# Optimization experiments

Measured on AMD Instinct MI355X. Metric: run time of the kernel, lower is better.

The kernel has to match this reference:

```python
import jax, jax.numpy as jnp
import numpy as np

# Multi-scale deformable attention (MSDeformAttn) with the pytorch grid_sample
# fallback semantics: bilinear, padding_mode='zeros', align_corners=False.
SPATIAL_SHAPES = [(128, 128), (64, 64), (32, 32), (16, 16)]  # (H_l, W_l)
N, C, M, L, P = 2, 256, 8, 4, 4
D = C // M
LEN_IN = sum(h * w for h, w in SPATIAL_SHAPES)  # 21760


def setup_inputs() -> dict:
    key = jax.random.key(0)
    ks = jax.random.split(key, 11)
    s = 0.02
    return {
        "query": jax.random.normal(ks[0], (N, LEN_IN, C), jnp.float32),
        "reference_points": jax.random.uniform(ks[1], (N, LEN_IN, L, 2), jnp.float32),
        "input_flatten": jax.random.normal(ks[2], (N, LEN_IN, C), jnp.float32),
        "W_off": jax.random.normal(ks[3], (C, M * L * P * 2), jnp.float32) * s,
        "b_off": jax.random.normal(ks[4], (M * L * P * 2,), jnp.float32) * s,
        "W_attn": jax.random.normal(ks[5], (C, M * L * P), jnp.float32) * s,
        "b_attn": jax.random.normal(ks[6], (M * L * P,), jnp.float32) * s,
        "W_val": jax.random.normal(ks[7], (C, C), jnp.float32) * s,
        "b_val": jax.random.normal(ks[8], (C,), jnp.float32) * s,
        "W_out": jax.random.normal(ks[9], (C, C), jnp.float32) * s,
        "b_out": jax.random.normal(ks[10], (C,), jnp.float32) * s,
    }


def _bilinear_sample(val_flat, gx, gy, H, W):
    """grid_sample(bilinear, zeros, align_corners=False) on one level.
    val_flat: (N, M, H*W, D); gx, gy: (N, M, Lq*P) in [-1, 1] (any value)."""
    x = (gx + 1.0) * (W * 0.5) - 0.5
    y = (gy + 1.0) * (H * 0.5) - 0.5
    x0 = jnp.floor(x)
    y0 = jnp.floor(y)
    wx1 = x - x0  # fractional parts
    wy1 = y - y0
    x0i = x0.astype(jnp.int32)
    y0i = y0.astype(jnp.int32)

    def gather(ix, iy):
        valid = (ix >= 0) & (ix < W) & (iy >= 0) & (iy < H)
        idx = jnp.clip(iy, 0, H - 1) * W + jnp.clip(ix, 0, W - 1)
        g = jnp.take_along_axis(val_flat, idx[..., None], axis=2)  # (N,M,LqP,D)
        return g * valid[..., None].astype(val_flat.dtype)

    g00 = gather(x0i, y0i)
    g01 = gather(x0i + 1, y0i)
    g10 = gather(x0i, y0i + 1)
    g11 = gather(x0i + 1, y0i + 1)
    return (g00 * ((1 - wx1) * (1 - wy1))[..., None]
            + g01 * (wx1 * (1 - wy1))[..., None]
            + g10 * ((1 - wx1) * wy1)[..., None]
            + g11 * (wx1 * wy1)[..., None])


def reference(query, reference_points, input_flatten, W_off, b_off,
              W_attn, b_attn, W_val, b_val, W_out, b_out):
    Nq, Lq, _ = query.shape
    # value projection -> (N, Len_in, M, D)
    value = (input_flatten @ W_val + b_val).reshape(Nq, -1, M, D)
    # sampling offsets -> (N, Lq, M, L, P, 2)
    offsets = (query @ W_off + b_off).reshape(Nq, Lq, M, L, P, 2)
    # attention weights: softmax over L*P
    attn = jax.nn.softmax((query @ W_attn + b_attn).reshape(Nq, Lq, M, L * P), axis=-1)
    attn = attn.reshape(Nq, Lq, M, L, P)
    # offset normalizer is (W_l, H_l)
    norm = jnp.array([[w, h] for h, w in SPATIAL_SHAPES], jnp.float32)  # (L, 2)
    loc = reference_points[:, :, None, :, None, :] + offsets / norm[None, None, None, :, None, :]
    grid = 2.0 * loc - 1.0  # (N, Lq, M, L, P, 2)

    acc = jnp.zeros((Nq, M, Lq, D), value.dtype)
    start = 0
    for lvl, (H, W) in enumerate(SPATIAL_SHAPES):
        val_flat = value[:, start:start + H * W].transpose(0, 2, 1, 3)  # (N,M,HW,D)
        gx = grid[:, :, :, lvl, :, 0].transpose(0, 2, 1, 3).reshape(Nq, M, Lq * P)
        gy = grid[:, :, :, lvl, :, 1].transpose(0, 2, 1, 3).reshape(Nq, M, Lq * P)
        samp = _bilinear_sample(val_flat, gx, gy, H, W).reshape(Nq, M, Lq, P, D)
        w_l = attn[:, :, :, lvl, :].transpose(0, 2, 1, 3)  # (N, M, Lq, P)
        acc = acc + jnp.einsum('nmqpd,nmqp->nmqd', samp, w_l)
        start += H * W

    out = acc.transpose(0, 2, 1, 3).reshape(Nq, Lq, C)  # (N, Lq, C)
    return out @ W_out + b_out
```

## Files before the change

kernel.cpp:

```cpp
#include <hip/hip_runtime.h>
#include <hip/hip_fp16.h>
#include <math.h>
#include <stdint.h>


constexpr int NB  = 2;
constexpr int C   = 256;
constexpr int M   = 8;
constexpr int D   = 32;
constexpr int LEN = 21760;
constexpr int QCHc = LEN / 2;

typedef __attribute__((ext_vector_type(8))) short short8v;
typedef __attribute__((ext_vector_type(4))) float f32x4;

__device__ __forceinline__ short f2bf(float x) {
  uint32_t u = __float_as_uint(x);
  u = (u + 0x7fffu + ((u >> 16) & 1u)) >> 16;
  return (short)u;
}

__global__ __launch_bounds__(256) void k_wpack(
    const float* __restrict__ Wval, const float* __restrict__ Woff,
    const float* __restrict__ Wattn, const float* __restrict__ Wout,
    short* __restrict__ WvP, short* __restrict__ WdP, short* __restrict__ WoP) {
  const int job = blockIdx.y;
  const int ncols = (job == 1) ? 384 : 256;
  const int NCG = ncols / 16;
  const int elems = 256 * ncols;
  const int idx = blockIdx.x * 256 + threadIdx.x;
  if (idx >= elems) return;
  const int e    = idx & 7;
  const int lane = (idx >> 3) & 63;
  const int lr = lane & 15, lk = lane >> 4;
  const int cgks = idx >> 9;
  const int cg = cgks % NCG, ks = cgks / NCG;
  const int k = ks * 32 + lk * 8 + e;
  const int col = cg * 16 + lr;
  float v;
  if (job == 0)      v = Wval[(size_t)k * 256 + col];
  else if (job == 2) v = Wout[(size_t)k * 256 + col];
  else               v = (col < 256) ? Woff[(size_t)k * 256 + col]
                                     : Wattn[(size_t)k * 128 + col - 256];
  short* dst = (job == 0) ? WvP : (job == 1) ? WdP : WoP;
  dst[idx] = f2bf(v);
}

__device__ __forceinline__ short8v ldBP(const short* __restrict__ WP, int NCG,
                                        int cg, int ks, int lane) {
  const int4 v = *(const int4*)(WP + ((size_t)((ks * NCG + cg) * 64 + lane)) * 8);
  union { int4 i; short8v s; } u; u.i = v; return u.s;
}

__device__ __forceinline__ void stage_cast(const float* __restrict__ p, char* sm, int t) {
  const int r = t >> 3, seg = t & 7;
  const float4* s = (const float4*)(p + (size_t)r * C + seg * 32);
  short v[32];
#pragma unroll
  for (int i = 0; i < 8; ++i) {
    float4 f = s[i];
    v[i * 4 + 0] = f2bf(f.x); v[i * 4 + 1] = f2bf(f.y);
    v[i * 4 + 2] = f2bf(f.z); v[i * 4 + 3] = f2bf(f.w);
  }
#pragma unroll
  for (int i = 0; i < 4; ++i) {
    const int kb = (seg * 32 + i * 8) * 2;
    *(int4*)(sm + r * 512 + (kb ^ ((r & 7) << 4))) = ((const int4*)v)[i];
  }
}

__device__ __forceinline__ void stage_bf16(const short* __restrict__ p, char* sm, int t) {
  const int r = t >> 3, seg = t & 7;
  const int4* s = (const int4*)(p + (size_t)r * C + seg * 32);
#pragma unroll
  for (int i = 0; i < 4; ++i) {
    const int kb = (seg * 32 + i * 8) * 2;
    *(int4*)(sm + r * 512 + (kb ^ ((r & 7) << 4))) = s[i];
  }
}

__device__ __forceinline__ short8v ldsA(const char* sm, int lane, int rt, int ks) {
  const int row = rt * 16 + (lane & 15);
  const int kb  = ks * 64 + ((lane >> 4) << 4);
  const int4 v = *(const int4*)(sm + row * 512 + (kb ^ ((row & 7) << 4)));
  union { int4 i; short8v s; } u; u.i = v; return u.s;
}

#define MFMA __builtin_amdgcn_mfma_f32_16x16x32_bf16

#define GEMM_BODY(WP)                                                       \
  short8v a[2][8];                                                          \
  _Pragma("unroll") for (int rt = 0; rt < 2; ++rt)                          \
  _Pragma("unroll") for (int ks = 0; ks < 8; ++ks)                          \
      a[rt][ks] = ldsA(smA, lane, rt, ks);                                  \
  f32x4 acc[2][4];                                                          \
  _Pragma("unroll") for (int rt = 0; rt < 2; ++rt)                          \
  _Pragma("unroll") for (int ct = 0; ct < 4; ++ct)                          \
      acc[rt][ct] = (f32x4){0.f, 0.f, 0.f, 0.f};                            \
  short8v b0[8], b1[8];                                                     \
  _Pragma("unroll") for (int ks = 0; ks < 8; ++ks)                          \
      b0[ks] = ldBP(WP, 16, cg0 + 0, ks, lane);                             \
  _Pragma("unroll") for (int ks = 0; ks < 8; ++ks)                          \
      b1[ks] = ldBP(WP, 16, cg0 + 1, ks, lane);                             \
  _Pragma("unroll") for (int ks = 0; ks < 8; ++ks) {                        \
    acc[0][0] = MFMA(a[0][ks], b0[ks], acc[0][0], 0, 0, 0);                 \
    acc[1][0] = MFMA(a[1][ks], b0[ks], acc[1][0], 0, 0, 0);                 \
  }                                                                         \
  _Pragma("unroll") for (int ks = 0; ks < 8; ++ks)                          \
      b0[ks] = ldBP(WP, 16, cg0 + 2, ks, lane);                             \
  _Pragma("unroll") for (int ks = 0; ks < 8; ++ks) {                        \
    acc[0][1] = MFMA(a[0][ks], b1[ks], acc[0][1], 0, 0, 0);                 \
    acc[1][1] = MFMA(a[1][ks], b1[ks], acc[1][1], 0, 0, 0);                 \
  }                                                                         \
  _Pragma("unroll") for (int ks = 0; ks < 8; ++ks)                          \
      b1[ks] = ldBP(WP, 16, cg0 + 3, ks, lane);                             \
  _Pragma("unroll") for (int ks = 0; ks < 8; ++ks) {                        \
    acc[0][2] = MFMA(a[0][ks], b0[ks], acc[0][2], 0, 0, 0);                 \
    acc[1][2] = MFMA(a[1][ks], b0[ks], acc[1][2], 0, 0, 0);                 \
  }                                                                         \
  _Pragma("unroll") for (int ks = 0; ks < 8; ++ks) {                        \
    acc[0][3] = MFMA(a[0][ks], b1[ks], acc[0][3], 0, 0, 0);                 \
    acc[1][3] = MFMA(a[1][ks], b1[ks], acc[1][3], 0, 0, 0);                 \
  }

__global__ __launch_bounds__(256, 2) void k_valproj(
    const float* __restrict__ infl, const short* __restrict__ WvP,
    const float* __restrict__ bv, __half* __restrict__ value) {
  __shared__ __align__(16) char smA[16384];
  const int t = threadIdx.x, lane = t & 63, w = t >> 6;
  const int r0 = blockIdx.x * 32;
  stage_cast(infl + (size_t)r0 * C, smA, t);
  __syncthreads();
  const int cg0 = w * 4;
  const int lr = lane & 15, lk = lane >> 4;
  GEMM_BODY(WvP)

  const int n = (blockIdx.x >= (LEN / 32)) ? 1 : 0;
  const int pixbase = r0 - n * LEN;
#pragma unroll
  for (int ct = 0; ct < 4; ++ct) {
    const int col = (cg0 + ct) * 16 + lr;
    const float bb = bv[col];
    const int m = col >> 5, d = col & 31;
    __half* vp = value + ((size_t)(n * 8 + m) * LEN) * 32 + d;
#pragma unroll
    for (int rt = 0; rt < 2; ++rt)
#pragma unroll
      for (int r = 0; r < 4; ++r) {
        const int pix = pixbase + rt * 16 + lk * 4 + r;
        vp[(size_t)pix * 32] = __float2half(acc[rt][ct][r] + bb);
      }
  }
}

__global__ __launch_bounds__(256, 2) void k_outproj(
    const short* __restrict__ accB, const short* __restrict__ WoP,
    const float* __restrict__ bo, float* __restrict__ out) {
  __shared__ __align__(16) char smA[16384];
  const int t = threadIdx.x, lane = t & 63, w = t >> 6;
  const int r0 = blockIdx.x * 32;
  stage_bf16(accB + (size_t)r0 * C, smA, t);
  __syncthreads();
  const int cg0 = w * 4;
  const int lr = lane & 15, lk = lane >> 4;
  GEMM_BODY(WoP)

#pragma unroll
  for (int ct = 0; ct < 4; ++ct) {
    const int col = (cg0 + ct) * 16 + lr;
    const float bb = bo[col];
#pragma unroll
    for (int rt = 0; rt < 2; ++rt)
#pragma unroll
      for (int r = 0; r < 4; ++r) {
        const int row = r0 + rt * 16 + lk * 4 + r;
        out[(size_t)row * C + col] = acc[rt][ct][r] + bb;
      }
  }
}

__global__ __launch_bounds__(256, 3) void k_desc(
    const float* __restrict__ query, const float* __restrict__ refp,
    const short* __restrict__ WdP, const float* __restrict__ boff,
    const float* __restrict__ battn, uint2* __restrict__ descD, int qbase) {
  __shared__ __align__(16) char smem[50176];
  char*  smA  = smem;
  float* offs = (float*)smem;
  float* attw = (float*)(smem + 32768);
  float* refs = (float*)(smem + 49152);

  const int t = threadIdx.x, lane = t & 63, w = t >> 6;
  const int n   = blockIdx.x / 340;
  const int q0c = (blockIdx.x % 340) * 32;
  const size_t qrow = (size_t)n * LEN + qbase + q0c;

  refs[t] = refp[qrow * 8 + t];
  stage_cast(query + qrow * C, smA, t);
  __syncthreads();

  f32x4 acc[2][6];
#pragma unroll
  for (int a = 0; a < 2; ++a)
#pragma unroll
    for (int b = 0; b < 6; ++b) acc[a][b] = (f32x4){0.f, 0.f, 0.f, 0.f};
  const int cgb = w * 6;
#pragma unroll
  for (int ks = 0; ks < 8; ++ks) {
    const short8v a0 = ldsA(smA, lane, 0, ks);
    const short8v a1 = ldsA(smA, lane, 1, ks);
#pragma unroll
    for (int ct = 0; ct < 6; ++ct) {
      const short8v b = ldBP(WdP, 24, cgb + ct, ks, lane);
      acc[0][ct] = MFMA(a0, b, acc[0][ct], 0, 0, 0);
      acc[1][ct] = MFMA(a1, b, acc[1][ct], 0, 0, 0);
    }
  }
  __syncthreads();

#pragma unroll
  for (int ct = 0; ct < 6; ++ct) {
    const int col = (cgb + ct) * 16 + (lane & 15);
    const float bb = (col < 256) ? boff[col] : battn[col - 256];
#pragma unroll
    for (int rt = 0; rt < 2; ++rt)
#pragma unroll
      for (int r = 0; r < 4; ++r) {
        const int row = rt * 16 + ((lane >> 4) << 2) + r;
        const float vv = acc[rt][ct][r] + bb;
        if (col < 256) offs[row * 256 + col] = vv;
        else           attw[row * 128 + col - 256] = vv;
      }
  }
  __syncthreads();

  {
    const int q = t >> 3, m = t & 7;
    float v[16], mx = -1e30f;
#pragma unroll
    for (int j = 0; j < 16; ++j) { v[j] = attw[q * 128 + m * 16 + j]; mx = fmaxf(mx, v[j]); }
    float s = 0.f;
#pragma unroll
    for (int j = 0; j < 16; ++j) { v[j] = __expf(v[j] - mx); s += v[j]; }
    const float inv = 1.f / s;
#pragma unroll
    for (int j = 0; j < 16; ++j) attw[q * 128 + m * 16 + j] = v[j] * inv;
  }
  __syncthreads();

#pragma unroll
  for (int i = 0; i < 16; ++i) {
    const int e = i * 256 + t;
    const int q = e >> 7, rem = e & 127;
    const int m = rem >> 4, j = rem & 15, l = j >> 2;
    const int jo = m * 16 + j;
    const float ox = offs[q * 256 + 2 * jo], oy = offs[q * 256 + 2 * jo + 1];
    const float aw = attw[q * 128 + jo];
    const float rx = refs[q * 8 + l * 2 + 0], ry = refs[q * 8 + l * 2 + 1];
    const int W = 128 >> l;
    const float x = rx * (float)W + ox - 0.5f;
    const float y = ry * (float)W + oy - 0.5f;
    const float xc = fminf(fmaxf(x, -8.f), 503.f);
    const float yc = fminf(fmaxf(y, -8.f), 503.f);
    const uint32_t xfix = (uint32_t)((xc + 8.f) * 128.f + 0.5f);
    const uint32_t yfix = (uint32_t)((yc + 8.f) * 128.f + 0.5f);
    uint2 dsc;
    dsc.x = xfix | (yfix << 16);
    dsc.y = (uint32_t)__half_as_ushort(__float2half_rn(aw));
    descD[((size_t)(n * 8 + m) * QCHc + q0c + q) * 16 + j] = dsc;
  }
}

__global__ __launch_bounds__(256, 4) void k_gather(
    const uint2* __restrict__ descD, const __half* __restrict__ value,
    short* __restrict__ accB, int qbase) {
  const int t = threadIdx.x;
  const int d4 = t & 3, ql = t >> 2;
  const int bid = blockIdx.x;
  const int s = bid & 15, qc = bid >> 4;
  const int n = s >> 3, m = s & 7;
  const int q = qc * 64 + ql;
  const uint4* dp4 = (const uint4*)(descD + ((size_t)(n * 8 + m) * QCHc + q) * 16);
  const char* vb = (const char*)value +
                   (size_t)((n * 8 + m) * LEN) * 64 + d4 * 16;

  uint4 dd[8];
#pragma unroll
  for (int i = 0; i < 8; ++i) dd[i] = dp4[i];
  __builtin_amdgcn_sched_barrier(0);

  float accf[8];
#pragma unroll
  for (int i = 0; i < 8; ++i) accf[i] = 0.f;

  union V { uint4 v; __half2 h[4]; };
  V rA[8], rB[8];
  __half2 hwA[8], hwB[8];

#define DECJ(G, ODD, R, HW, BASE)                                             \
  {                                                                           \
    constexpr int l_ = (G) >> 1;                                              \
    constexpr int W_ = 128 >> l_;                                             \
    constexpr int stl_ = (l_ == 0) ? 0 : (l_ == 1) ? 16384 : (l_ == 2) ? 20480 : 21504; \
    const uint32_t lo_ = (ODD) ? dd[G].z : dd[G].x;                           \
    const uint32_t hi_ = (ODD) ? dd[G].w : dd[G].y;                           \
    const int xf_ = (int)(lo_ & 0xffffu), yf_ = (int)(lo_ >> 16);             \
    const float aw_ = __half2float(__ushort_as_half((unsigned short)(hi_ & 0xffffu))); \
    const int xi_ = (xf_ >> 7) - 8, yi_ = (yf_ >> 7) - 8;                     \
    const float fx_ = (float)(xf_ & 127) * 0.0078125f;                        \
    const float fy_ = (float)(yf_ & 127) * 0.0078125f;                        \
    float wx0_ = 1.f - fx_, wx1_ = fx_, wy0_ = 1.f - fy_, wy1_ = fy_;         \
    if (xi_ < 0 || xi_ >= W_)         wx0_ = 0.f;                             \
    if (xi_ + 1 < 0 || xi_ + 1 >= W_) wx1_ = 0.f;                             \
    if (yi_ < 0 || yi_ >= W_)         wy0_ = 0.f;                             \
    if (yi_ + 1 < 0 || yi_ + 1 >= W_) wy1_ = 0.f;                             \
    const int x0_ = min(max(xi_, 0), W_ - 1), x1_ = min(max(xi_ + 1, 0), W_ - 1); \
    const int y0_ = min(max(yi_, 0), W_ - 1), y1_ = min(max(yi_ + 1, 0), W_ - 1); \
    HW[(BASE) + 0] = __float2half2_rn(wx0_ * wy0_ * aw_);                     \
    HW[(BASE) + 1] = __float2half2_rn(wx1_ * wy0_ * aw_);                     \
    HW[(BASE) + 2] = __float2half2_rn(wx0_ * wy1_ * aw_);                     \
    HW[(BASE) + 3] = __float2half2_rn(wx1_ * wy1_ * aw_);                     \
    R[(BASE) + 0].v = *(const uint4*)(vb + (size_t)(stl_ + y0_ * W_ + x0_) * 64u); \
    R[(BASE) + 1].v = *(const uint4*)(vb + (size_t)(stl_ + y0_ * W_ + x1_) * 64u); \
    R[(BASE) + 2].v = *(const uint4*)(vb + (size_t)(stl_ + y1_ * W_ + x0_) * 64u); \
    R[(BASE) + 3].v = *(const uint4*)(vb + (size_t)(stl_ + y1_ * W_ + x1_) * 64u); \
  }

#define DECG(G, R, HW)                                                        \
  DECJ(G, 0, R, HW, 0)                                                        \
  DECJ(G, 1, R, HW, 4)                                                        \
  __builtin_amdgcn_sched_barrier(0);

#define CONSG(R, HW)                                                          \
  {                                                                           \
    __half2 acch[4];                                                          \
    _Pragma("unroll") for (int i_ = 0; i_ < 4; ++i_)                          \
        acch[i_] = __float2half2_rn(0.f);                                     \
    _Pragma("unroll") for (int c_ = 0; c_ < 8; ++c_) {                        \
      _Pragma("unroll") for (int i_ = 0; i_ < 4; ++i_)                        \
          acch[i_] = __hfma2(R[c_].h[i_], HW[c_], acch[i_]);                  \
    }                                                                         \
    _Pragma("unroll") for (int i_ = 0; i_ < 4; ++i_) {                        \
      const float2 f_ = __half22float2(acch[i_]);                             \
      accf[2 * i_] += f_.x; accf[2 * i_ + 1] += f_.y;                         \
    }                                                                         \
  }

  DECG(0, rA, hwA)
  DECG(1, rB, hwB)
  CONSG(rA, hwA)
  DECG(2, rA, hwA)
  CONSG(rB, hwB)
  DECG(3, rB, hwB)
  CONSG(rA, hwA)
  DECG(4, rA, hwA)
  CONSG(rB, hwB)
  DECG(5, rB, hwB)
  CONSG(rA, hwA)
  DECG(6, rA, hwA)
  CONSG(rB, hwB)
  DECG(7, rB, hwB)
  CONSG(rA, hwA)
  CONSG(rB, hwB)
#undef DECJ
#undef DECG
#undef CONSG

  short8v o;
#pragma unroll
  for (int i = 0; i < 8; ++i) o[i] = f2bf(accf[i]);
  *(short8v*)(accB + ((size_t)n * LEN + qbase + q) * 256 + m * 32 + d4 * 8) = o;
}

extern "C" void kernel_launch(void* const* d_in, const int* in_sizes, int n_in,
                              void* d_out, int out_size, void* d_ws, size_t ws_size,
                              hipStream_t stream) {
  const float* query = (const float*)d_in[0];
  const float* refp  = (const float*)d_in[1];
  const float* infl  = (const float*)d_in[2];
  const float* Woff  = (const float*)d_in[3];
  const float* boff  = (const float*)d_in[4];
  const float* Wattn = (const float*)d_in[5];
  const float* battn = (const float*)d_in[6];
  const float* Wval  = (const float*)d_in[7];
  const float* bval  = (const float*)d_in[8];
  const float* Wout  = (const float*)d_in[9];
  const float* bout  = (const float*)d_in[10];
  float* out = (float*)d_out;

  char* ws = (char*)d_ws;
  __half* value = (__half*)ws;
  short*  accB  = (short*)(ws + 22282240);
  uint2*  desc8 = (uint2*)(ws + 44564480);
  short*  WvP   = (short*)(ws + 66846720);
  short*  WdP   = (short*)(ws + 66977792);
  short*  WoP   = (short*)(ws + 67174400);

  k_wpack<<<dim3(384, 3), 256, 0, stream>>>(Wval, Woff, Wattn, Wout,
                                            WvP, WdP, WoP);

  k_valproj<<<(NB * LEN) / 32, 256, 0, stream>>>(infl, WvP, bval, value);

  for (int c = 0; c < 2; ++c) {
    k_desc<<<NB * (QCHc / 32), 256, 0, stream>>>(query, refp, WdP, boff, battn,
                                                 desc8, c * QCHc);
    k_gather<<<16 * (QCHc / 64), 256, 0, stream>>>(desc8, value, accB, c * QCHc);
  }

  k_outproj<<<(NB * LEN) / 32, 256, 0, stream>>>(accB, WoP, bout, out);
}
```

Measured before the change: 156.8 us.

## Pad value maps with a zero border to drop bilinear bounds checks

Value projection now writes each level's feature map into a buffer with a one-pixel zero border, filled by a new k_zpad kernel. The descriptor builder clamps coordinates to [-1, W] instead of [-8, 503], so the gather kernel can drop the per-corner validity tests and index clamping. Each sample now loads two adjacent pixel pairs at fixed offsets from one base address. This cuts ALU work in the gather loop, in exchange for an extra small launch, a slightly larger value buffer, and scattered store addresses in valproj.

```diff
diff --git a/kernel.cpp b/kernel.cpp
--- a/kernel.cpp
+++ b/kernel.cpp
@@ -10,6 +10,7 @@
 constexpr int D   = 32;
 constexpr int LEN = 21760;
 constexpr int QCHc = LEN / 2;
+constexpr int PADPIX = 22736;
 
 typedef __attribute__((ext_vector_type(8))) short short8v;
 typedef __attribute__((ext_vector_type(4))) float f32x4;
@@ -44,6 +45,23 @@
                                      : Wattn[(size_t)k * 128 + col - 256];
   short* dst = (job == 0) ? WvP : (job == 1) ? WdP : WoP;
   dst[idx] = f2bf(v);
+}
+
+__global__ __launch_bounds__(256) void k_zpad(__half* __restrict__ value) {
+  const int s = blockIdx.x, l = blockIdx.y;
+  const int Wp  = (l == 0) ? 130 : (l == 1) ? 66 : (l == 2) ? 34 : 18;
+  const int stp = (l == 0) ? 0 : (l == 1) ? 16900 : (l == 2) ? 21256 : 22412;
+  const int cells = 4 * Wp - 4;
+  const uint4 z = {0u, 0u, 0u, 0u};
+  char* base = (char*)value + (size_t)s * PADPIX * 64;
+  for (int i = threadIdx.x; i < cells * 4; i += 256) {
+    const int cell = i >> 2, d4 = i & 3;
+    int row, col;
+    if (cell < Wp)            { row = 0;       col = cell; }
+    else if (cell < 2 * Wp)   { row = Wp - 1;  col = cell - Wp; }
+    else { const int c2 = cell - 2 * Wp; row = 1 + (c2 >> 1); col = (c2 & 1) ? (Wp - 1) : 0; }
+    *(uint4*)(base + (size_t)(stp + row * Wp + col) * 64 + d4 * 16) = z;
+  }
 }
 
 __device__ __forceinline__ short8v ldBP(const short* __restrict__ WP, int NCG,
@@ -137,19 +155,32 @@
 
   const int n = (blockIdx.x >= (LEN / 32)) ? 1 : 0;
   const int pixbase = r0 - n * LEN;
+
+  int pidx8[2][4];
+#pragma unroll
+  for (int rt = 0; rt < 2; ++rt)
+#pragma unroll
+    for (int r = 0; r < 4; ++r) {
+      const int pix = pixbase + rt * 16 + lk * 4 + r;
+      int pi;
+      if (pix < 16384)      { const int y = pix >> 7;           pi = (y + 1) * 130 + (pix & 127) + 1; }
+      else if (pix < 20480) { const int y = (pix - 16384) >> 6; pi = 16900 + (y + 1) * 66 + (pix & 63) + 1; }
+      else if (pix < 21504) { const int y = (pix - 20480) >> 5; pi = 21256 + (y + 1) * 34 + (pix & 31) + 1; }
+      else                  { const int y = (pix - 21504) >> 4; pi = 22412 + (y + 1) * 18 + (pix & 15) + 1; }
+      pidx8[rt][r] = pi;
+    }
+
 #pragma unroll
   for (int ct = 0; ct < 4; ++ct) {
     const int col = (cg0 + ct) * 16 + lr;
     const float bb = bv[col];
     const int m = col >> 5, d = col & 31;
-    __half* vp = value + ((size_t)(n * 8 + m) * LEN) * 32 + d;
+    __half* vp = value + ((size_t)(n * 8 + m) * PADPIX) * 32 + d;
 #pragma unroll
     for (int rt = 0; rt < 2; ++rt)
 #pragma unroll
-      for (int r = 0; r < 4; ++r) {
-        const int pix = pixbase + rt * 16 + lk * 4 + r;
-        vp[(size_t)pix * 32] = __float2half(acc[rt][ct][r] + bb);
-      }
+      for (int r = 0; r < 4; ++r)
+        vp[(size_t)pidx8[rt][r] * 32] = __float2half(acc[rt][ct][r] + bb);
   }
 }
 
@@ -257,12 +288,13 @@
     const float aw = attw[q * 128 + jo];
     const float rx = refs[q * 8 + l * 2 + 0], ry = refs[q * 8 + l * 2 + 1];
     const int W = 128 >> l;
-    const float x = rx * (float)W + ox - 0.5f;
-    const float y = ry * (float)W + oy - 0.5f;
-    const float xc = fminf(fmaxf(x, -8.f), 503.f);
-    const float yc = fminf(fmaxf(y, -8.f), 503.f);
-    const uint32_t xfix = (uint32_t)((xc + 8.f) * 128.f + 0.5f);
-    const uint32_t yfix = (uint32_t)((yc + 8.f) * 128.f + 0.5f);
+    const float fW = (float)W;
+    const float x = rx * fW + ox - 0.5f;
+    const float y = ry * fW + oy - 0.5f;
+    const float xc = fminf(fmaxf(x, -1.f), fW);
+    const float yc = fminf(fmaxf(y, -1.f), fW);
+    const uint32_t xfix = (uint32_t)((xc + 1.f) * 128.f + 0.5f);
+    const uint32_t yfix = (uint32_t)((yc + 1.f) * 128.f + 0.5f);
     uint2 dsc;
     dsc.x = xfix | (yfix << 16);
     dsc.y = (uint32_t)__half_as_ushort(__float2half_rn(aw));
@@ -281,7 +313,7 @@
   const int q = qc * 64 + ql;
   const uint4* dp4 = (const uint4*)(descD + ((size_t)(n * 8 + m) * QCHc + q) * 16);
   const char* vb = (const char*)value +
-                   (size_t)((n * 8 + m) * LEN) * 64 + d4 * 16;
+                   (size_t)((n * 8 + m)) * PADPIX * 64 + d4 * 16;
 
   uint4 dd[8];
 #pragma unroll
@@ -300,29 +332,28 @@
   {                                                                           \
     constexpr int l_ = (G) >> 1;                                              \
     constexpr int W_ = 128 >> l_;                                             \
-    constexpr int stl_ = (l_ == 0) ? 0 : (l_ == 1) ? 16384 : (l_ == 2) ? 20480 : 21504; \
+    constexpr int Wp_ = W_ + 2;                                               \
+    constexpr int stp_ = (l_ == 0) ? 0 : (l_ == 1) ? 16900 : (l_ == 2) ? 21256 : 22412; \
     const uint32_t lo_ = (ODD) ? dd[G].z : dd[G].x;                           \
     const uint32_t hi_ = (ODD) ? dd[G].w : dd[G].y;                           \
     const int xf_ = (int)(lo_ & 0xffffu), yf_ = (int)(lo_ >> 16);             \
     const float aw_ = __half2float(__ushort_as_half((unsigned short)(hi_ & 0xffffu))); \
-    const int xi_ = (xf_ >> 7) - 8, yi_ = (yf_ >> 7) - 8;                     \
+    const int xi_ = xf_ >> 7, yi_ = yf_ >> 7;                                 \
     const float fx_ = (float)(xf_ & 127) * 0.0078125f;                        \
     const float fy_ = (float)(yf_ & 127) * 0.0078125f;                        \
-    float wx0_ = 1.f - fx_, wx1_ = fx_, wy0_ = 1.f - fy_, wy1_ = fy_;         \
-    if (xi_ < 0 || xi_ >= W_)         wx0_ = 0.f;                             \
-    if (xi_ + 1 < 0 || xi_ + 1 >= W_) wx1_ = 0.f;                             \
-    if (yi_ < 0 || yi_ >= W_)         wy0_ = 0.f;                             \
-    if (yi_ + 1 < 0 || yi_ + 1 >= W_) wy1_ = 0.f;                             \
-    const int x0_ = min(max(xi_, 0), W_ - 1), x1_ = min(max(xi_ + 1, 0), W_ - 1); \
-    const int y0_ = min(max(yi_, 0), W_ - 1), y1_ = min(max(yi_ + 1, 0), W_ - 1); \
-    HW[(BASE) + 0] = __float2half2_rn(wx0_ * wy0_ * aw_);                     \
-    HW[(BASE) + 1] = __float2half2_rn(wx1_ * wy0_ * aw_);                     \
-    HW[(BASE) + 2] = __float2half2_rn(wx0_ * wy1_ * aw_);                     \
-    HW[(BASE) + 3] = __float2half2_rn(wx1_ * wy1_ * aw_);                     \
-    R[(BASE) + 0].v = *(const uint4*)(vb + (size_t)(stl_ + y0_ * W_ + x0_) * 64u); \
-    R[(BASE) + 1].v = *(const uint4*)(vb + (size_t)(stl_ + y0_ * W_ + x1_) * 64u); \
-    R[(BASE) + 2].v = *(const uint4*)(vb + (size_t)(stl_ + y1_ * W_ + x0_) * 64u); \
-    R[(BASE) + 3].v = *(const uint4*)(vb + (size_t)(stl_ + y1_ * W_ + x1_) * 64u); \
+    const float wx0_ = 1.f - fx_;                                             \
+    const float wy0a_ = (1.f - fy_) * aw_;                                    \
+    const float wy1a_ = fy_ * aw_;                                            \
+    HW[(BASE) + 0] = __float2half2_rn(wx0_ * wy0a_);                          \
+    HW[(BASE) + 1] = __float2half2_rn(fx_ * wy0a_);                           \
+    HW[(BASE) + 2] = __float2half2_rn(wx0_ * wy1a_);                          \
+    HW[(BASE) + 3] = __float2half2_rn(fx_ * wy1a_);                           \
+    const char* a0_ = vb + (size_t)(stp_ + yi_ * Wp_ + xi_) * 64u;            \
+    const char* a1_ = a0_ + Wp_ * 64;                                         \
+    R[(BASE) + 0].v = *(const uint4*)(a0_);                                   \
+    R[(BASE) + 1].v = *(const uint4*)(a0_ + 64);                              \
+    R[(BASE) + 2].v = *(const uint4*)(a1_);                                   \
+    R[(BASE) + 3].v = *(const uint4*)(a1_ + 64);                              \
   }
 
 #define DECG(G, R, HW)                                                        \
@@ -389,14 +420,15 @@
 
   char* ws = (char*)d_ws;
   __half* value = (__half*)ws;
-  short*  accB  = (short*)(ws + 22282240);
-  uint2*  desc8 = (uint2*)(ws + 44564480);
-  short*  WvP   = (short*)(ws + 66846720);
-  short*  WdP   = (short*)(ws + 66977792);
-  short*  WoP   = (short*)(ws + 67174400);
+  short*  accB  = (short*)(ws + 23281664);
+  uint2*  desc8 = (uint2*)(ws + 45563904);
+  short*  WvP   = (short*)(ws + 67846144);
+  short*  WdP   = (short*)(ws + 67977216);
+  short*  WoP   = (short*)(ws + 68173824);
 
   k_wpack<<<dim3(384, 3), 256, 0, stream>>>(Wval, Woff, Wattn, Wout,
                                             WvP, WdP, WoP);
+  k_zpad<<<dim3(16, 4), 256, 0, stream>>>(value);
 
   k_valproj<<<(NB * LEN) / 32, 256, 0, stream>>>(infl, WvP, bval, value);
 
```

Result: no change. 154.5 us (-1.4%).
